# Optimization experiments

Measured on AMD Instinct MI355X. Metric: run time of the kernel, lower is better.

## Reference

```python
import jax, jax.numpy as jnp
import numpy as np

D_MODEL = 1024
N_HEADS = 16
D_HEAD = D_MODEL // N_HEADS


def setup_inputs() -> dict:
    key = jax.random.key(0)
    k_x, k_qkv, k_out = jax.random.split(key, 3)
    x = jax.random.normal(k_x, (2, 2048, D_MODEL), dtype=jnp.float32)
    # nn.Linear weights: out = x @ W.T ; store as [out_features, in_features]
    s = 1.0 / np.sqrt(D_MODEL)
    w_qkv = jax.random.uniform(k_qkv, (3 * D_MODEL, D_MODEL), jnp.float32, -s, s)
    w_out = jax.random.uniform(k_out, (D_MODEL, D_MODEL), jnp.float32, -s, s)
    return {"x": x, "w_qkv": w_qkv, "w_out": w_out}


def reference(x, w_qkv, w_out):
    B, T, D = x.shape
    qkv = jnp.einsum("btd,ed->bte", x, w_qkv)  # [B,T,3D]
    q, k, v = jnp.split(qkv, 3, axis=-1)

    def heads(t):  # [B,T,D] -> [B,H,T,d]
        return t.reshape(B, T, N_HEADS, D_HEAD).transpose(0, 2, 1, 3)

    q, k, v = heads(q), heads(k), heads(v)
    scale = jnp.float32(np.sqrt(D_HEAD))
    scores = jnp.einsum("bhqd,bhkd->bhqk", q, k) / scale  # [B,H,T,T]
    causal = jnp.tril(jnp.ones((T, T), dtype=bool))  # True = keep
    scores = jnp.where(causal, scores, -jnp.inf)
    attn = jax.nn.softmax(scores, axis=-1)
    out = jnp.einsum("bhqk,bhkd->bhqd", attn, v)
    out = out.transpose(0, 2, 1, 3).reshape(B, T, D)
    return jnp.einsum("btd,ed->bte", out, w_out)
```

## Files before the change

### kernel.cpp

```cpp
#include <hip/hip_runtime.h>
#include <hip/hip_bf16.h>

typedef __attribute__((ext_vector_type(8))) short bf16x8;
typedef __attribute__((ext_vector_type(8))) unsigned short ushort8;
typedef __attribute__((ext_vector_type(4))) float f32x4;
typedef __attribute__((ext_vector_type(16))) float f32x16;

typedef const __attribute__((address_space(1))) void gvoid;
typedef __attribute__((address_space(3))) void svoid;

__device__ __forceinline__ unsigned short f2bf(float f) {
  union { float f; unsigned int u; } v; v.f = f;
  unsigned int u = v.u;
  unsigned int r = (u + 0x7fffu + ((u >> 16) & 1u)) >> 16;
  return (unsigned short)r;
}
__device__ __forceinline__ float bf2f(unsigned short u) {
  union { unsigned int i; float f; } v; v.i = ((unsigned int)u) << 16; return v.f;
}

__global__ void cast3_kernel(const float* __restrict__ a, int na4,
                             const float* __restrict__ b, int nb4,
                             const float* __restrict__ c, int nc4,
                             unsigned short* __restrict__ oa,
                             unsigned short* __restrict__ ob,
                             unsigned short* __restrict__ oc) {
  const int total = na4 + nb4 + nc4;
  for (int i = blockIdx.x * 256 + threadIdx.x; i < total; i += gridDim.x * 256) {
    const float* src; unsigned short* dst; int j = i;
    if (j < na4) { src = a; dst = oa; }
    else if (j < na4 + nb4) { j -= na4; src = b; dst = ob; }
    else { j -= na4 + nb4; src = c; dst = oc; }
    const float4 v = reinterpret_cast<const float4*>(src)[j];
    ushort4 o4;
    o4.x = f2bf(v.x); o4.y = f2bf(v.y); o4.z = f2bf(v.z); o4.w = f2bf(v.w);
    reinterpret_cast<ushort4*>(dst)[j] = o4;
  }
}

template<bool OUT_BF16>
__global__ __launch_bounds__(256) void gemm_bt(const unsigned short* __restrict__ A,
                                               const unsigned short* __restrict__ B,
                                               void* __restrict__ Cv,
                                               int M, int N, int K,
                                               float qscale, int qcols) {
  constexpr int BM = 128, BK = 32, TILE = BM * BK;
  __shared__ alignas(16) unsigned short As[2 * TILE];
  __shared__ alignas(16) unsigned short Bs[2 * TILE];
  const int tid = threadIdx.x;
  const int l  = tid & 63;
  const int w  = tid >> 6;
  const int wr = w >> 1, wc = w & 1;
  const int lr = l & 15, lg = l >> 4;
  const long tile_m = (long)blockIdx.x * BM;
  const long tile_n = (long)blockIdx.y * BM;

  const int c0 = tid, c1 = tid + 256;
  const unsigned short* pa0 = A + (tile_m + (c0 >> 2)) * (long)K + (c0 & 3) * 8;
  const unsigned short* pa1 = A + (tile_m + (c1 >> 2)) * (long)K + (c1 & 3) * 8;
  const unsigned short* pb0 = B + (tile_n + (c0 >> 2)) * (long)K + (c0 & 3) * 8;
  const unsigned short* pb1 = B + (tile_n + (c1 >> 2)) * (long)K + (c1 & 3) * 8;
  const int woff = w * 512;

  f32x4 acc[4][4] = {};

  __builtin_amdgcn_global_load_lds((gvoid*)pa0, (svoid*)(As + woff), 16, 0, 0);
  __builtin_amdgcn_global_load_lds((gvoid*)pa1, (svoid*)(As + 2048 + woff), 16, 0, 0);
  __builtin_amdgcn_global_load_lds((gvoid*)pb0, (svoid*)(Bs + woff), 16, 0, 0);
  __builtin_amdgcn_global_load_lds((gvoid*)pb1, (svoid*)(Bs + 2048 + woff), 16, 0, 0);
  __syncthreads();

  int cur = 0;
  for (int k0 = 0; k0 < K; k0 += BK) {
    if (k0 + BK < K) {
      unsigned short* An = As + (cur ^ 1) * TILE;
      unsigned short* Bn = Bs + (cur ^ 1) * TILE;
      __builtin_amdgcn_global_load_lds((gvoid*)(pa0 + k0 + BK), (svoid*)(An + woff), 16, 0, 0);
      __builtin_amdgcn_global_load_lds((gvoid*)(pa1 + k0 + BK), (svoid*)(An + 2048 + woff), 16, 0, 0);
      __builtin_amdgcn_global_load_lds((gvoid*)(pb0 + k0 + BK), (svoid*)(Bn + woff), 16, 0, 0);
      __builtin_amdgcn_global_load_lds((gvoid*)(pb1 + k0 + BK), (svoid*)(Bn + 2048 + woff), 16, 0, 0);
    }
    const unsigned short* AsC = As + cur * TILE;
    const unsigned short* BsC = Bs + cur * TILE;
    bf16x8 af[4], bfr[4];
#pragma unroll
    for (int m = 0; m < 4; ++m)
      af[m] = *reinterpret_cast<const bf16x8*>(AsC + (wr * 64 + m * 16 + lr) * BK + lg * 8);
#pragma unroll
    for (int n = 0; n < 4; ++n)
      bfr[n] = *reinterpret_cast<const bf16x8*>(BsC + (wc * 64 + n * 16 + lr) * BK + lg * 8);
#pragma unroll
    for (int m = 0; m < 4; ++m)
#pragma unroll
      for (int n = 0; n < 4; ++n)
        acc[m][n] = __builtin_amdgcn_mfma_f32_16x16x32_bf16(af[m], bfr[n], acc[m][n], 0, 0, 0);
    __syncthreads();
    cur ^= 1;
  }

#pragma unroll
  for (int m = 0; m < 4; ++m)
#pragma unroll
    for (int n = 0; n < 4; ++n)
#pragma unroll
      for (int r = 0; r < 4; ++r) {
        long row = tile_m + wr * 64 + m * 16 + lg * 4 + r;
        long col = tile_n + wc * 64 + n * 16 + lr;
        float sc = (col < qcols) ? qscale : 1.0f;
        if (OUT_BF16)
          reinterpret_cast<unsigned short*>(Cv)[row * N + col] = f2bf(acc[m][n][r] * sc);
        else
          reinterpret_cast<float*>(Cv)[row * N + col] = acc[m][n][r] * sc;
      }
}

__global__ __launch_bounds__(256, 2) void attn_kernel(const unsigned short* __restrict__ qkv,
                                                      unsigned short* __restrict__ o,
                                                      unsigned short* __restrict__ Opart,
                                                      float* __restrict__ mpart,
                                                      float* __restrict__ lpart) {
  constexpr int E = 3072, T = 2048;
  __shared__ alignas(16) unsigned short Ks[64 * 64];
  __shared__ alignas(16) unsigned short Vt[64 * 64];
  __shared__ float alBuf[4][32];

  static const int jq[24]  = {15,15, 7,14,14,13,13, 6,12,12,11,11, 5,10,10, 9, 9, 4, 8, 8, 3, 2, 1, 0};
  static const int jt0[24] = { 0,16, 0, 0,15, 0,14, 0, 0,13, 0,12, 0, 0,11, 0,10, 0, 0, 9, 0, 0, 0, 0};
  static const int jt1[24] = {16,32,16,15,30,14,28,14,13,26,12,24,12,11,22,10,20,10, 9,18, 8, 6, 4, 2};

  const int tid = threadIdx.x;
  const int l = tid & 63, w = tid >> 6;
  const int hh = l >> 5;
  const int lc = l & 31;
  int jj = blockIdx.x >> 5;
  if (jj >= 8 && jj < 16) jj = 23 - jj;
  const int bh = blockIdx.x & 31;
  const int qtb = jq[jj], t0 = jt0[jj], t1 = jt1[jj];
  const bool isSplit = (qtb >= 8);
  const int part = (t0 != 0) ? 1 : 0;
  const int pidx = (((bh << 3) + (qtb - 8)) << 1) + part;
  const int b = bh >> 4, hd = bh & 15;
  const unsigned short* Qb = qkv + (size_t)b * T * E + hd * 64;
  const unsigned short* Kb = Qb + 1024;
  const unsigned short* Vb = Qb + 2048;

  const int qrow0 = qtb * 128 + w * 32;
  const int qg = qrow0 + lc;

  const int kr0 = tid >> 3, js0 = tid & 7;
  const int kr1 = kr0 + 32;
  const unsigned short* sK = Kb + (size_t)kr0 * E + js0 * 8;
  const unsigned short* sV = Vb + (size_t)kr0 * E + js0 * 8;
  const size_t tileStep = (size_t)64 * E;

  bf16x8 aq[4];
#pragma unroll
  for (int c = 0; c < 4; ++c)
    aq[c] = *reinterpret_cast<const bf16x8*>(Qb + (size_t)qg * E + c * 16 + hh * 8);

  f32x16 accO0 = {}, accO1 = {};
  float mL = -1e30f, ls = 0.f;

  ushort8 k0 = *reinterpret_cast<const ushort8*>(sK + (size_t)t0 * tileStep);
  ushort8 k1 = *reinterpret_cast<const ushort8*>(sK + (size_t)t0 * tileStep + 32 * E);
  ushort8 v0 = *reinterpret_cast<const ushort8*>(sV + (size_t)t0 * tileStep);
  ushort8 v1 = *reinterpret_cast<const ushort8*>(sV + (size_t)t0 * tileStep + 32 * E);

  for (int t = t0; t < t1; ++t) {
    __syncthreads();
    *reinterpret_cast<ushort8*>(Ks + kr0 * 64 + ((js0 ^ (kr0 & 7)) << 3)) = k0;
    *reinterpret_cast<ushort8*>(Ks + kr1 * 64 + ((js0 ^ (kr1 & 7)) << 3)) = k1;
#pragma unroll
    for (int e = 0; e < 8; ++e) {
      int d = js0 * 8 + e;
      int swz = (d ^ (d >> 3)) & 7;
      Vt[d * 64 + ((((kr0 >> 3) ^ swz) << 3) | (kr0 & 7))] = (unsigned short)v0[e];
      Vt[d * 64 + ((((kr1 >> 3) ^ swz) << 3) | (kr1 & 7))] = (unsigned short)v1[e];
    }
    __syncthreads();
    if (t + 1 < t1) {
      const unsigned short* nK = sK + (size_t)(t + 1) * tileStep;
      const unsigned short* nV = sV + (size_t)(t + 1) * tileStep;
      k0 = *reinterpret_cast<const ushort8*>(nK);
      k1 = *reinterpret_cast<const ushort8*>(nK + 32 * E);
      v0 = *reinterpret_cast<const ushort8*>(nV);
      v1 = *reinterpret_cast<const ushort8*>(nV + 32 * E);
    }

    if (t * 64 > qrow0 + 31) continue;

    f32x16 sT0 = {}, sT1 = {};
    __builtin_amdgcn_s_setprio(1);
#pragma unroll
    for (int c = 0; c < 4; ++c) {
      int sl = ((2 * c + hh) ^ (lc & 7)) << 3;
      bf16x8 ak0 = *reinterpret_cast<const bf16x8*>(Ks + lc * 64 + sl);
      bf16x8 ak1 = *reinterpret_cast<const bf16x8*>(Ks + (32 + lc) * 64 + sl);
      sT0 = __builtin_amdgcn_mfma_f32_32x32x16_bf16(ak0, aq[c], sT0, 0, 0, 0);
      sT1 = __builtin_amdgcn_mfma_f32_32x32x16_bf16(ak1, aq[c], sT1, 0, 0, 0);
    }
    __builtin_amdgcn_s_setprio(0);

    const bool needMask = (t * 64 + 63) > qrow0;
    float pm = -1e30f;
    if (needMask) {
#pragma unroll
      for (int r = 0; r < 16; ++r) {
        int kb = t * 64 + (r & 3) + 8 * (r >> 2) + 4 * hh;
        float a0 = sT0[r], a1 = sT1[r];
        if (kb > qg) a0 = -1e30f;
        if (kb + 32 > qg) a1 = -1e30f;
        sT0[r] = a0; sT1[r] = a1;
        pm = fmaxf(pm, fmaxf(a0, a1));
      }
    } else {
#pragma unroll
      for (int r = 0; r < 16; ++r)
        pm = fmaxf(pm, fmaxf(sT0[r], sT1[r]));
    }
    pm = fmaxf(pm, __shfl_xor(pm, 32));

    if (__any(pm > mL + 8.f)) {
      float mn = fmaxf(mL, pm);
      float al = __expf(mL - mn);
      mL = mn;
      ls *= al;
      alBuf[w][lc] = al;
      asm volatile("s_waitcnt lgkmcnt(0)" ::: "memory");
      __builtin_amdgcn_sched_barrier(0);
#pragma unroll
      for (int r = 0; r < 16; ++r) {
        float alr = alBuf[w][(r & 3) + 8 * (r >> 2) + 4 * hh];
        accO0[r] *= alr;
        accO1[r] *= alr;
      }
    }

    bf16x8 pa[4];
    union U4 { unsigned int u[4]; bf16x8 v; };
#pragma unroll
    for (int n = 0; n < 2; ++n) {
      float p[16];
#pragma unroll
      for (int r = 0; r < 16; ++r) {
        float pv = __expf((n ? sT1[r] : sT0[r]) - mL);
        p[r] = pv;
        ls += pv;
      }
#pragma unroll
      for (int gg = 0; gg < 2; ++gg) {
        unsigned int x0, x1, y0, y1;
        asm("v_cvt_pk_bf16_f32 %0, %1, %2" : "=v"(x0) : "v"(p[8 * gg + 0]), "v"(p[8 * gg + 1]));
        asm("v_cvt_pk_bf16_f32 %0, %1, %2" : "=v"(x1) : "v"(p[8 * gg + 2]), "v"(p[8 * gg + 3]));
        asm("v_cvt_pk_bf16_f32 %0, %1, %2" : "=v"(y0) : "v"(p[8 * gg + 4]), "v"(p[8 * gg + 5]));
        asm("v_cvt_pk_bf16_f32 %0, %1, %2" : "=v"(y1) : "v"(p[8 * gg + 6]), "v"(p[8 * gg + 7]));
        asm("v_permlane32_swap_b32 %0, %1" : "+v"(x0), "+v"(y0));
        asm("v_permlane32_swap_b32 %0, %1" : "+v"(x1), "+v"(y1));
        U4 fu;
        fu.u[0] = x0; fu.u[1] = x1; fu.u[2] = y0; fu.u[3] = y1;
        pa[2 * n + gg] = fu.v;
      }
    }

    __builtin_amdgcn_s_setprio(1);
#pragma unroll
    for (int cp = 0; cp < 4; ++cp) {
      int d0 = lc, d1 = 32 + lc;
      int sl0 = ((2 * cp + hh) ^ ((d0 ^ (d0 >> 3)) & 7)) << 3;
      int sl1 = ((2 * cp + hh) ^ ((d1 ^ (d1 >> 3)) & 7)) << 3;
      bf16x8 bv0 = *reinterpret_cast<const bf16x8*>(Vt + d0 * 64 + sl0);
      bf16x8 bv1 = *reinterpret_cast<const bf16x8*>(Vt + d1 * 64 + sl1);
      accO0 = __builtin_amdgcn_mfma_f32_32x32x16_bf16(pa[cp], bv0, accO0, 0, 0, 0);
      accO1 = __builtin_amdgcn_mfma_f32_32x32x16_bf16(pa[cp], bv1, accO1, 0, 0, 0);
    }
    __builtin_amdgcn_s_setprio(0);
  }

  float lsT = ls + __shfl_xor(ls, 32);
  if (isSplit) {
    if (hh == 0) {
      mpart[pidx * 128 + w * 32 + lc] = mL;
      lpart[pidx * 128 + w * 32 + lc] = lsT;
    }
#pragma unroll
    for (int r = 0; r < 16; ++r) {
      int q = (r & 3) + 8 * (r >> 2) + 4 * hh;
      int rp = w * 32 + q;
      Opart[(size_t)pidx * 8192 + rp * 64 + lc]      = f2bf(accO0[r]);
      Opart[(size_t)pidx * 8192 + rp * 64 + 32 + lc] = f2bf(accO1[r]);
    }
  } else {
    float inv = 1.f / lsT;
    alBuf[w][lc] = inv;
    asm volatile("s_waitcnt lgkmcnt(0)" ::: "memory");
    __builtin_amdgcn_sched_barrier(0);
#pragma unroll
    for (int r = 0; r < 16; ++r) {
      int q = (r & 3) + 8 * (r >> 2) + 4 * hh;
      float iv = alBuf[w][q];
      size_t row = (size_t)(b * T + qrow0 + q) * 1024 + hd * 64;
      o[row + lc]      = f2bf(accO0[r] * iv);
      o[row + 32 + lc] = f2bf(accO1[r] * iv);
    }
  }
}

__global__ __launch_bounds__(256) void merge_kernel(const unsigned short* __restrict__ Opart,
                                                    const float* __restrict__ mpart,
                                                    const float* __restrict__ lpart,
                                                    unsigned short* __restrict__ o) {
  const int e = blockIdx.x * 256 + threadIdx.x;
  const int rowid = e >> 3, c8 = e & 7;
  const int bh = rowid >> 10, rem = rowid & 1023;
  const int q8 = rem >> 7, r = rem & 127;
  const int b = bh >> 4, hd = bh & 15;
  const int p0 = (((bh << 3) + q8) << 1);
  const float m0 = mpart[p0 * 128 + r], m1 = mpart[(p0 + 1) * 128 + r];
  const float l0 = lpart[p0 * 128 + r], l1 = lpart[(p0 + 1) * 128 + r];
  const float mS = fmaxf(m0, m1);
  const float e0 = __expf(m0 - mS), e1 = __expf(m1 - mS);
  const float inv = 1.f / (l0 * e0 + l1 * e1);
  const float f0 = e0 * inv, f1 = e1 * inv;
  const ushort8 a = *reinterpret_cast<const ushort8*>(Opart + (size_t)p0 * 8192 + r * 64 + c8 * 8);
  const ushort8 bb = *reinterpret_cast<const ushort8*>(Opart + (size_t)(p0 + 1) * 8192 + r * 64 + c8 * 8);
  ushort8 out;
#pragma unroll
  for (int j = 0; j < 8; ++j)
    out[j] = f2bf(bf2f(a[j]) * f0 + bf2f(bb[j]) * f1);
  const size_t row = (size_t)(b * 2048 + (q8 + 8) * 128 + r) * 1024 + hd * 64 + c8 * 8;
  *reinterpret_cast<ushort8*>(o + row) = out;
}

extern "C" void kernel_launch(void* const* d_in, const int* in_sizes, int n_in,
                              void* d_out, int out_size, void* d_ws, size_t ws_size,
                              hipStream_t stream) {
  const float* x     = (const float*)d_in[0];
  const float* w_qkv = (const float*)d_in[1];
  const float* w_out = (const float*)d_in[2];
  float* out = (float*)d_out;

  unsigned short* xb    = (unsigned short*)d_ws;
  unsigned short* wqkvb = xb    + (size_t)4096 * 1024;
  unsigned short* woutb = wqkvb + (size_t)3072 * 1024;
  unsigned short* qkv   = woutb + (size_t)1024 * 1024;
  unsigned short* attn  = qkv   + (size_t)4096 * 3072;

  unsigned short* Opart = xb;
  float* mpart = (float*)wqkvb;
  float* lpart = mpart + 512 * 128;

  cast3_kernel<<<dim3(2048), 256, 0, stream>>>(x,     4096 * 1024 / 4,
                                               w_qkv, 3072 * 1024 / 4,
                                               w_out, 1024 * 1024 / 4,
                                               xb, wqkvb, woutb);

  gemm_bt<true ><<<dim3(32, 24), 256, 0, stream>>>(xb,   wqkvb, (void*)qkv,  4096, 3072, 1024,
                                                   0.125f, 1024);
  attn_kernel  <<<dim3(768), 256, 0, stream>>>(qkv, attn, Opart, mpart, lpart);
  merge_kernel <<<dim3(1024), 256, 0, stream>>>(Opart, mpart, lpart, attn);
  gemm_bt<false><<<dim3(32,  8), 256, 0, stream>>>(attn, woutb, (void*)out, 4096, 1024, 1024,
                                                   1.0f, 0);
}
```

Before: 105.4 us.

## Rebalance causal attention split-K schedule into 32 work slots per head

Replaces the 24-slot causal work schedule with a 32-slot table that splits query tiles 5–10 into two KV chunks and tiles 11–15 into three, so each block does a more even amount of KV work and the grid grows from 768 to 1024 blocks. The first partial of each split tile is written directly into the attention output buffer rather than a separate partial buffer, and the merge kernel now combines two or three partials. This aims to cut tail imbalance and fill more CUs, at the cost of more partial writes and a larger merge pass.

Result: slower. 111.0 us (+5.2%).

```diff
diff --git a/kernel.cpp b/kernel.cpp
--- a/kernel.cpp
+++ b/kernel.cpp
@@ -124,21 +124,32 @@
   __shared__ alignas(16) unsigned short Vt[64 * 64];
   __shared__ float alBuf[4][32];
 
-  static const int jq[24]  = {15,15, 7,14,14,13,13, 6,12,12,11,11, 5,10,10, 9, 9, 4, 8, 8, 3, 2, 1, 0};
-  static const int jt0[24] = { 0,16, 0, 0,15, 0,14, 0, 0,13, 0,12, 0, 0,11, 0,10, 0, 0, 9, 0, 0, 0, 0};
-  static const int jt1[24] = {16,32,16,15,30,14,28,14,13,26,12,24,12,11,22,10,20,10, 9,18, 8, 6, 4, 2};
+  static const int jq[32]  = {10,15,15, 9,14,13,13, 8,
+                              10,15, 9,14,14,13,12, 8,
+                               4, 3, 7, 7,11,11,12,12,
+                               0, 1, 2, 5, 5, 6, 6,11};
+  static const int jt0[32] = { 0, 0,22,10,10, 0,19, 0,
+                              11,11, 0, 0,20,10, 0, 9,
+                               0, 0, 0, 8, 0, 8, 9,18,
+                               0, 0, 0, 0, 6, 0, 7,16};
+  static const int jt1[32] = {11,11,32,20,20,10,28, 9,
+                              22,22,10,10,30,19, 9,18,
+                              10, 8, 8,16, 8,16,18,26,
+                               2, 4, 6, 6,12, 7,14,24};
+  static const int jp[32]  = { 0, 0, 2, 1, 1, 0, 2, 0,
+                               1, 1, 0, 0, 2, 1, 0, 1,
+                              -1,-1, 0, 1, 0, 1, 1, 2,
+                              -1,-1,-1, 0, 1, 0, 1, 2};
 
   const int tid = threadIdx.x;
   const int l = tid & 63, w = tid >> 6;
   const int hh = l >> 5;
   const int lc = l & 31;
-  int jj = blockIdx.x >> 5;
-  if (jj >= 8 && jj < 16) jj = 23 - jj;
+  const int jj = blockIdx.x >> 5;
   const int bh = blockIdx.x & 31;
   const int qtb = jq[jj], t0 = jt0[jj], t1 = jt1[jj];
-  const bool isSplit = (qtb >= 8);
-  const int part = (t0 != 0) ? 1 : 0;
-  const int pidx = (((bh << 3) + (qtb - 8)) << 1) + part;
+  const int part = jp[jj];
+  const bool isSplit = (part >= 0);
   const int b = bh >> 4, hd = bh & 15;
   const unsigned short* Qb = qkv + (size_t)b * T * E + hd * 64;
   const unsigned short* Kb = Qb + 1024;
@@ -278,16 +289,30 @@
 
   float lsT = ls + __shfl_xor(ls, 32);
   if (isSplit) {
+    const int mlIdx = bh * 27 + ((qtb < 11) ? (qtb - 5) * 2 + part
+                                            : 12 + (qtb - 11) * 3 + part);
     if (hh == 0) {
-      mpart[pidx * 128 + w * 32 + lc] = mL;
-      lpart[pidx * 128 + w * 32 + lc] = lsT;
-    }
-#pragma unroll
-    for (int r = 0; r < 16; ++r) {
-      int q = (r & 3) + 8 * (r >> 2) + 4 * hh;
-      int rp = w * 32 + q;
-      Opart[(size_t)pidx * 8192 + rp * 64 + lc]      = f2bf(accO0[r]);
-      Opart[(size_t)pidx * 8192 + rp * 64 + 32 + lc] = f2bf(accO1[r]);
+      mpart[mlIdx * 128 + w * 32 + lc] = mL;
+      lpart[mlIdx * 128 + w * 32 + lc] = lsT;
+    }
+    if (part == 0) {
+#pragma unroll
+      for (int r = 0; r < 16; ++r) {
+        int q = (r & 3) + 8 * (r >> 2) + 4 * hh;
+        size_t row = (size_t)(b * T + qrow0 + q) * 1024 + hd * 64;
+        o[row + lc]      = f2bf(accO0[r]);
+        o[row + 32 + lc] = f2bf(accO1[r]);
+      }
+    } else {
+      const int opIdx = bh * 16 + ((qtb < 11) ? (qtb - 5)
+                                              : 6 + (qtb - 11) * 2 + (part - 1));
+#pragma unroll
+      for (int r = 0; r < 16; ++r) {
+        int q = (r & 3) + 8 * (r >> 2) + 4 * hh;
+        int rp = w * 32 + q;
+        Opart[(size_t)opIdx * 8192 + rp * 64 + lc]      = f2bf(accO0[r]);
+        Opart[(size_t)opIdx * 8192 + rp * 64 + 32 + lc] = f2bf(accO1[r]);
+      }
     }
   } else {
     float inv = 1.f / lsT;
@@ -311,23 +336,41 @@
                                                     unsigned short* __restrict__ o) {
   const int e = blockIdx.x * 256 + threadIdx.x;
   const int rowid = e >> 3, c8 = e & 7;
-  const int bh = rowid >> 10, rem = rowid & 1023;
-  const int q8 = rem >> 7, r = rem & 127;
+  const int bh = rowid / 1408;
+  const int rem = rowid - bh * 1408;
+  const int qs = rem >> 7, r = rem & 127;
+  const int qtb = 5 + qs;
   const int b = bh >> 4, hd = bh & 15;
-  const int p0 = (((bh << 3) + q8) << 1);
-  const float m0 = mpart[p0 * 128 + r], m1 = mpart[(p0 + 1) * 128 + r];
-  const float l0 = lpart[p0 * 128 + r], l1 = lpart[(p0 + 1) * 128 + r];
-  const float mS = fmaxf(m0, m1);
+  const int np = (qtb < 11) ? 2 : 3;
+  const int mlBase = bh * 27 + ((qtb < 11) ? (qtb - 5) * 2 : 12 + (qtb - 11) * 3);
+  const int opBase = bh * 16 + ((qtb < 11) ? (qtb - 5) : 6 + (qtb - 11) * 2);
+
+  float m0 = mpart[(mlBase + 0) * 128 + r];
+  float m1 = mpart[(mlBase + 1) * 128 + r];
+  float mS = fmaxf(m0, m1);
+  float m2 = -1e30f;
+  if (np == 3) { m2 = mpart[(mlBase + 2) * 128 + r]; mS = fmaxf(mS, m2); }
   const float e0 = __expf(m0 - mS), e1 = __expf(m1 - mS);
-  const float inv = 1.f / (l0 * e0 + l1 * e1);
-  const float f0 = e0 * inv, f1 = e1 * inv;
-  const ushort8 a = *reinterpret_cast<const ushort8*>(Opart + (size_t)p0 * 8192 + r * 64 + c8 * 8);
-  const ushort8 bb = *reinterpret_cast<const ushort8*>(Opart + (size_t)(p0 + 1) * 8192 + r * 64 + c8 * 8);
+  const float e2 = (np == 3) ? __expf(m2 - mS) : 0.f;
+  float L = lpart[(mlBase + 0) * 128 + r] * e0 + lpart[(mlBase + 1) * 128 + r] * e1;
+  if (np == 3) L += lpart[(mlBase + 2) * 128 + r] * e2;
+  const float inv = 1.f / L;
+  const float f0 = e0 * inv, f1 = e1 * inv, f2 = e2 * inv;
+
+  const size_t row = (size_t)(b * 2048 + qtb * 128 + r) * 1024 + hd * 64 + c8 * 8;
+  const ushort8 a0 = *reinterpret_cast<const ushort8*>(o + row);
+  const ushort8 a1 = *reinterpret_cast<const ushort8*>(Opart + (size_t)(opBase + 0) * 8192 + r * 64 + c8 * 8);
   ushort8 out;
-#pragma unroll
-  for (int j = 0; j < 8; ++j)
-    out[j] = f2bf(bf2f(a[j]) * f0 + bf2f(bb[j]) * f1);
-  const size_t row = (size_t)(b * 2048 + (q8 + 8) * 128 + r) * 1024 + hd * 64 + c8 * 8;
+  if (np == 3) {
+    const ushort8 a2 = *reinterpret_cast<const ushort8*>(Opart + (size_t)(opBase + 1) * 8192 + r * 64 + c8 * 8);
+#pragma unroll
+    for (int j = 0; j < 8; ++j)
+      out[j] = f2bf(bf2f(a0[j]) * f0 + bf2f(a1[j]) * f1 + bf2f(a2[j]) * f2);
+  } else {
+#pragma unroll
+    for (int j = 0; j < 8; ++j)
+      out[j] = f2bf(bf2f(a0[j]) * f0 + bf2f(a1[j]) * f1);
+  }
   *reinterpret_cast<ushort8*>(o + row) = out;
 }
 
@@ -347,7 +390,7 @@
 
   unsigned short* Opart = xb;
   float* mpart = (float*)wqkvb;
-  float* lpart = mpart + 512 * 128;
+  float* lpart = mpart + 864 * 128;
 
   cast3_kernel<<<dim3(2048), 256, 0, stream>>>(x,     4096 * 1024 / 4,
                                                w_qkv, 3072 * 1024 / 4,
@@ -356,8 +399,8 @@
 
   gemm_bt<true ><<<dim3(32, 24), 256, 0, stream>>>(xb,   wqkvb, (void*)qkv,  4096, 3072, 1024,
                                                    0.125f, 1024);
-  attn_kernel  <<<dim3(768), 256, 0, stream>>>(qkv, attn, Opart, mpart, lpart);
-  merge_kernel <<<dim3(1024), 256, 0, stream>>>(Opart, mpart, lpart, attn);
+  attn_kernel  <<<dim3(1024), 256, 0, stream>>>(qkv, attn, Opart, mpart, lpart);
+  merge_kernel <<<dim3(1408), 256, 0, stream>>>(Opart, mpart, lpart, attn);
   gemm_bt<false><<<dim3(32,  8), 256, 0, stream>>>(attn, woutb, (void*)out, 4096, 1024, 1024,
                                                    1.0f, 0);
 }
```

## Use 256x256-tile 512-thread GEMM with direct global-to-LDS loads for QKV projection

Applied to the files above, without the earlier changes.

Adds a new bf16 MFMA GEMM kernel with 256x256 output tiles, 8 waves, BK=64 double-buffered LDS staging through global_load_lds with an XOR swizzle. It replaces the 128x128 GEMM for the QKV projection. The aim is more operand reuse per block and fewer LDS round trips through registers. The trade-off is only 192 blocks on a 256-CU part and large LDS usage per block.

Result: slower. 108.8 us (+3.2%).

```diff
diff --git a/kernel.cpp b/kernel.cpp
--- a/kernel.cpp
+++ b/kernel.cpp
@@ -36,6 +36,104 @@
     o4.x = f2bf(v.x); o4.y = f2bf(v.y); o4.z = f2bf(v.z); o4.w = f2bf(v.w);
     reinterpret_cast<ushort4*>(dst)[j] = o4;
   }
+}
+
+template<bool OUT_BF16>
+__global__ __launch_bounds__(512, 2) void gemm256(const unsigned short* __restrict__ A,
+                                                  const unsigned short* __restrict__ B,
+                                                  void* __restrict__ Cv,
+                                                  int M, int N, int K,
+                                                  float qscale, int qcols) {
+  __shared__ alignas(16) unsigned short As[2][2][128 * 64];
+  __shared__ alignas(16) unsigned short Bs[2][2][128 * 64];
+  const int tid = threadIdx.x;
+  const int l = tid & 63, w = tid >> 6;
+  const int lr = l & 15, lg = l >> 4;
+  const int wm = w >> 2, wn = w & 3;
+  const long tm = (long)blockIdx.x * 256;
+  const long tn = (long)blockIdx.y * 256;
+
+  const int srow = tid >> 3;
+  const int gslot = (tid & 7) ^ (srow & 7);
+  const unsigned short* gA = A + (tm + srow) * (long)K + gslot * 8;
+  const unsigned short* gB = B + (tn + srow) * (long)K + gslot * 8;
+  const int dstOff = 512 * w;
+
+  f32x4 acc[8][4] = {};
+
+  const long rowK64 = 64 * (long)K, rowK128 = 128 * (long)K, rowK192 = 192 * (long)K;
+
+#define STAGE256(buf, kt)                                                                           \
+  {                                                                                                 \
+    const long ko = (long)(kt) * 64;                                                                \
+    __builtin_amdgcn_global_load_lds((gvoid*)(gA + ko),           (svoid*)(&As[buf][0][dstOff]), 16, 0, 0);        \
+    __builtin_amdgcn_global_load_lds((gvoid*)(gA + rowK64 + ko),  (svoid*)(&As[buf][0][4096 + dstOff]), 16, 0, 0); \
+    __builtin_amdgcn_global_load_lds((gvoid*)(gA + rowK128 + ko), (svoid*)(&As[buf][1][dstOff]), 16, 0, 0);        \
+    __builtin_amdgcn_global_load_lds((gvoid*)(gA + rowK192 + ko), (svoid*)(&As[buf][1][4096 + dstOff]), 16, 0, 0); \
+    __builtin_amdgcn_global_load_lds((gvoid*)(gB + ko),           (svoid*)(&Bs[buf][0][dstOff]), 16, 0, 0);        \
+    __builtin_amdgcn_global_load_lds((gvoid*)(gB + rowK64 + ko),  (svoid*)(&Bs[buf][0][4096 + dstOff]), 16, 0, 0); \
+    __builtin_amdgcn_global_load_lds((gvoid*)(gB + rowK128 + ko), (svoid*)(&Bs[buf][1][dstOff]), 16, 0, 0);        \
+    __builtin_amdgcn_global_load_lds((gvoid*)(gB + rowK192 + ko), (svoid*)(&Bs[buf][1][4096 + dstOff]), 16, 0, 0); \
+  }
+
+  const int NT = K >> 6;
+  STAGE256(0, 0);
+  STAGE256(1, 1);
+  asm volatile("s_waitcnt vmcnt(8)" ::: "memory");
+  __builtin_amdgcn_s_barrier();
+  __builtin_amdgcn_sched_barrier(0);
+
+  int cur = 0;
+  for (int kt = 0; kt < NT; ++kt) {
+    const unsigned short* Ah = &As[cur][wm][0];
+    const unsigned short* Bh = &Bs[cur][wn >> 1][(wn & 1) * 4096];
+#pragma unroll
+    for (int kk = 0; kk < 2; ++kk) {
+      bf16x8 af[8], bfv[4];
+      const int sl = ((kk * 4 + lg) ^ (lr & 7)) << 3;
+#pragma unroll
+      for (int m = 0; m < 8; ++m)
+        af[m] = *reinterpret_cast<const bf16x8*>(Ah + (m * 16 + lr) * 64 + sl);
+#pragma unroll
+      for (int n = 0; n < 4; ++n)
+        bfv[n] = *reinterpret_cast<const bf16x8*>(Bh + (n * 16 + lr) * 64 + sl);
+#pragma unroll
+      for (int m = 0; m < 8; ++m)
+#pragma unroll
+        for (int n = 0; n < 4; ++n)
+          acc[m][n] = __builtin_amdgcn_mfma_f32_16x16x32_bf16(af[m], bfv[n], acc[m][n], 0, 0, 0);
+    }
+    asm volatile("s_waitcnt lgkmcnt(0)" ::: "memory");
+    __builtin_amdgcn_s_barrier();
+    __builtin_amdgcn_sched_barrier(0);
+    if (kt + 1 < NT) {
+      if (kt + 2 < NT) {
+        STAGE256(cur, kt + 2);
+        asm volatile("s_waitcnt vmcnt(8)" ::: "memory");
+      } else {
+        asm volatile("s_waitcnt vmcnt(0)" ::: "memory");
+      }
+      __builtin_amdgcn_s_barrier();
+      __builtin_amdgcn_sched_barrier(0);
+    }
+    cur ^= 1;
+  }
+#undef STAGE256
+
+#pragma unroll
+  for (int m = 0; m < 8; ++m)
+#pragma unroll
+    for (int n = 0; n < 4; ++n)
+#pragma unroll
+      for (int r = 0; r < 4; ++r) {
+        long row = tm + wm * 128 + m * 16 + lg * 4 + r;
+        long col = tn + wn * 64 + n * 16 + lr;
+        float sc = (col < qcols) ? qscale : 1.0f;
+        if (OUT_BF16)
+          reinterpret_cast<unsigned short*>(Cv)[row * N + col] = f2bf(acc[m][n][r] * sc);
+        else
+          reinterpret_cast<float*>(Cv)[row * N + col] = acc[m][n][r] * sc;
+      }
 }
 
 template<bool OUT_BF16>
@@ -354,10 +452,10 @@
                                                w_out, 1024 * 1024 / 4,
                                                xb, wqkvb, woutb);
 
-  gemm_bt<true ><<<dim3(32, 24), 256, 0, stream>>>(xb,   wqkvb, (void*)qkv,  4096, 3072, 1024,
-                                                   0.125f, 1024);
+  gemm256<true><<<dim3(16, 12), 512, 0, stream>>>(xb, wqkvb, (void*)qkv, 4096, 3072, 1024,
+                                                  0.125f, 1024);
   attn_kernel  <<<dim3(768), 256, 0, stream>>>(qkv, attn, Opart, mpart, lpart);
   merge_kernel <<<dim3(1024), 256, 0, stream>>>(Opart, mpart, lpart, attn);
-  gemm_bt<false><<<dim3(32,  8), 256, 0, stream>>>(attn, woutb, (void*)out, 4096, 1024, 1024,
-                                                   1.0f, 0);
-}
+  gemm_bt<false><<<dim3(32, 8), 256, 0, stream>>>(attn, woutb, (void*)out, 4096, 1024, 1024,
+                                                  1.0f, 0);
+}
```
